# Kernel optimization log

Hardware: AMD Instinct MI355X
Metric: run time of the kernel (lower is better)

Reference implementation:

```python
import jax, jax.numpy as jnp
import numpy as np

N_SYS = 512      # number of crystal systems in the batch
N_ATOM = 32      # atoms per system (uniform for the reference)
N = N_SYS * N_ATOM            # 16384 total atoms
M = N_SYS * N_ATOM * N_ATOM   # 524288 dense intra-system edges
R = 16           # lattice translation points per edge
E = 128          # embed_dim
H = 8            # num_heads


def setup_inputs() -> dict:
    key = jax.random.key(0)
    ks = jax.random.split(key, 6)
    x = jax.random.normal(ks[0], (N, E), jnp.float32)
    in_proj_weight = jax.random.normal(ks[1], (3 * E, E), jnp.float32) / np.float32(np.sqrt(E))
    in_proj_bias = jnp.zeros((3 * E,), jnp.float32)
    out_proj_weight = jax.random.normal(ks[2], (E, E), jnp.float32) / np.float32(np.sqrt(E))
    out_proj_bias = jnp.zeros((E,), jnp.float32)
    # per-node per-head Gaussian exponents; must be negative for convergent lattice sums
    alpha = -(jax.random.uniform(ks[3], (N, H), jnp.float32) * 0.9 + 0.1)
    # squared distances from atom i to lattice images of atom j, up to ~5 Angstrom
    dist2 = jax.random.uniform(ks[4], (M, R), jnp.float32) * 25.0
    # dense intra-system edge list in (query-major) block order, as Crystalformer assumes
    base = (np.arange(N_SYS, dtype=np.int32) * N_ATOM)[:, None, None]
    qi = np.arange(N_ATOM, dtype=np.int32)[None, :, None]
    kj = np.arange(N_ATOM, dtype=np.int32)[None, None, :]
    e0 = np.broadcast_to(base + qi, (N_SYS, N_ATOM, N_ATOM)).reshape(-1)
    e1 = np.broadcast_to(base + kj, (N_SYS, N_ATOM, N_ATOM)).reshape(-1)
    edges = jnp.asarray(np.stack([e0, e1]), jnp.int32)
    batch = jnp.asarray(np.repeat(np.arange(N_SYS, dtype=np.int32), N_ATOM))
    return {
        "x": x,
        "in_proj_weight": in_proj_weight,
        "in_proj_bias": in_proj_bias,
        "out_proj_weight": out_proj_weight,
        "out_proj_bias": out_proj_bias,
        "alpha": alpha,
        "dist2": dist2,
        "edges": edges,
        "batch": batch,
    }


def reference(x, in_proj_weight, in_proj_bias, out_proj_weight, out_proj_bias,
              alpha, dist2, edges, batch):
    n, e = x.shape
    h = alpha.shape[1]
    dh = e // h
    # in-projection (self-attention: q = k = v = x)
    qkv = x @ in_proj_weight.T + in_proj_bias           # [N, 3E]
    q, k, v = jnp.split(qkv, 3, axis=-1)
    q = q.reshape(n, h, dh) / jnp.sqrt(jnp.asarray(dh, x.dtype))
    k = k.reshape(n, h, dh)
    v = v.reshape(n, h, dh)
    e0, e1 = edges[0], edges[1]
    # per-edge dot-product score, gathered q/k  -> [M, H]
    attn = jnp.einsum("mhd,mhd->mh", q[e0], k[e1])
    # real-domain lattice-sum attention bias: logsumexp_r(alpha_i * |r|^2)  -> [M, H]
    aw = jax.nn.logsumexp(alpha[e0][:, :, None] * dist2[:, None, :], axis=-1)
    s = attn + aw
    # segment softmax over each query's neighborhood (norm_func_mode=0 'default')
    smax = jax.ops.segment_max(s, e0, num_segments=n)   # [N, H]
    p = jnp.exp(s - smax[e0])
    denom = jax.ops.segment_sum(p, e0, num_segments=n)  # [N, H]
    p = p / denom[e0]
    # scatter-add aggregation of gathered values  -> [N, H, dh]
    out = jax.ops.segment_sum(p[:, :, None] * v[e1], e0, num_segments=n)
    # out-projection
    out = out.reshape(n, e) @ out_proj_weight.T + out_proj_bias
    return out
```

## Files before the change

kernel.cpp:

```cpp
#include <hip/hip_runtime.h>
#include <hip/hip_bf16.h>

#define LOG2E_F 1.4426950408889634f

typedef __attribute__((ext_vector_type(8))) short short8;
typedef __attribute__((ext_vector_type(4))) float f32x4;
typedef __attribute__((ext_vector_type(2))) float f32x2;

__device__ inline unsigned short f2b(float f) {
    __hip_bfloat16 h = __float2bfloat16(f);
    return *reinterpret_cast<unsigned short*>(&h);
}

__device__ inline short8 load_frag_f32(const float* p) {
    const float4 lo = *(const float4*)p;
    const float4 hi = *(const float4*)(p + 4);
    short8 r;
    r[0] = (short)f2b(lo.x); r[1] = (short)f2b(lo.y);
    r[2] = (short)f2b(lo.z); r[3] = (short)f2b(lo.w);
    r[4] = (short)f2b(hi.x); r[5] = (short)f2b(hi.y);
    r[6] = (short)f2b(hi.z); r[7] = (short)f2b(hi.w);
    return r;
}

__device__ inline f32x2 mk2(float a, float b) { f32x2 r; r.x = a; r.y = b; return r; }
__device__ inline f32x2 bfup(unsigned u) {
    return mk2(__uint_as_float(u << 16), __uint_as_float(u & 0xffff0000u));
}
#define PK_FMA(a, b, c) __builtin_elementwise_fma((a), (b), (c))

__global__ __launch_bounds__(256) void prep_kernel(
    const float* __restrict__ x, const float* __restrict__ Win,
    const float* __restrict__ Wout,
    unsigned short* __restrict__ xbf, unsigned short* __restrict__ winbf,
    unsigned short* __restrict__ woutbf)
{
    const int i = blockIdx.x * 256 + threadIdx.x;
    const float* src; unsigned short* dst; size_t off;
    if (i < 262144)       { src = x;    dst = xbf;    off = (size_t)i * 8; }
    else if (i < 268288)  { src = Win;  dst = winbf;  off = (size_t)(i - 262144) * 8; }
    else                  { src = Wout; dst = woutbf; off = (size_t)(i - 268288) * 8; }
    const short8 r = load_frag_f32(src + off);
    *(short8*)(dst + off) = r;
}

__global__ __launch_bounds__(512, 2) void fused2_kernel(
    const unsigned short* __restrict__ xbf, const unsigned short* __restrict__ winbf,
    const float* __restrict__ bin, const unsigned short* __restrict__ woutbf,
    const float* __restrict__ bout, const float* __restrict__ alpha,
    const float* __restrict__ dist2, float* __restrict__ out)
{
    __shared__ float qf[2][32][164];
    __shared__ unsigned short kvb[2][2][32][8][16];
    __shared__ unsigned short aggb[2][32][136];

    const int tid  = threadIdx.x;
    const int g    = tid >> 8;
    const int t    = tid & 255;
    const int sys  = blockIdx.x * 2 + g;
    const int lane = t & 63;
    const int wv   = t >> 6;
    const int r16  = lane & 15;
    const int kg   = lane >> 4;
    const int base = sys << 5;

    short8 af[2][4];
    #pragma unroll
    for (int rt = 0; rt < 2; ++rt)
        #pragma unroll
        for (int ks = 0; ks < 4; ++ks)
            af[rt][ks] = *(const short8*)(
                xbf + (size_t)(base + rt * 16 + r16) * 128 + ks * 32 + kg * 8);

    #pragma unroll
    for (int j = 0; j < 6; ++j) {
        const int ct = wv * 6 + j;
        const int c  = ct * 16 + r16;
        short8 bf[4];
        #pragma unroll
        for (int ks = 0; ks < 4; ++ks)
            bf[ks] = *(const short8*)(winbf + (size_t)c * 128 + ks * 32 + kg * 8);
        const float bias_v = bin[c];
        const int   bufi   = ct >> 3;
        const int   hh     = ct & 7;

        #pragma unroll
        for (int rt = 0; rt < 2; ++rt) {
            f32x4 acc = {0.f, 0.f, 0.f, 0.f};
            #pragma unroll
            for (int ks = 0; ks < 4; ++ks)
                acc = __builtin_amdgcn_mfma_f32_16x16x32_bf16(af[rt][ks], bf[ks], acc, 0, 0, 0);
            #pragma unroll
            for (int r = 0; r < 4; ++r) {
                const int atom = rt * 16 + kg * 4 + r;
                const float v  = acc[r] + bias_v;
                if (bufi == 0)
                    qf[g][atom][hh * 20 + r16] = v * (0.25f * LOG2E_F);
                else
                    kvb[g][bufi - 1][atom][hh][r16] = f2b(v);
            }
        }
    }

    const int qi = t >> 3;
    const int h  = t & 7;
    const float al2 = alpha[(size_t)(base + qi) * 8 + h] * LOG2E_F;
    const f32x2 al22 = mk2(al2, al2);

    __syncthreads();

    f32x2 q2[8];
    {
        const float* qrow = &qf[g][qi][h * 20];
        #pragma unroll
        for (int d4 = 0; d4 < 4; ++d4) {
            const float4 tq = *(const float4*)(qrow + (d4 << 2));
            q2[d4 * 2 + 0] = mk2(tq.x, tq.y);
            q2[d4 * 2 + 1] = mk2(tq.z, tq.w);
        }
    }

    float den = 0.f;
    f32x2 acc2[8] = {};
    const float* dp = dist2 + (size_t)(sys * 1024 + qi * 32) * 16;

    #pragma unroll 4
    for (int kj = 0; kj < 32; ++kj, dp += 16) {
        const float4 t0 = *(const float4*)(dp + 0);
        const float4 t1 = *(const float4*)(dp + 4);
        const float4 t2 = *(const float4*)(dp + 8);
        const float4 t3 = *(const float4*)(dp + 12);
        const f32x2 d2p[8] = {mk2(t0.x,t0.y), mk2(t0.z,t0.w), mk2(t1.x,t1.y), mk2(t1.z,t1.w),
                              mk2(t2.x,t2.y), mk2(t2.z,t2.w), mk2(t3.x,t3.y), mk2(t3.z,t3.w)};
        f32x2 es;
        {
            const f32x2 a0 = al22 * d2p[0];
            es = mk2(__builtin_amdgcn_exp2f(a0.x), __builtin_amdgcn_exp2f(a0.y));
            #pragma unroll
            for (int i = 1; i < 8; ++i) {
                const f32x2 a = al22 * d2p[i];
                es += mk2(__builtin_amdgcn_exp2f(a.x), __builtin_amdgcn_exp2f(a.y));
            }
        }
        const float ssum = es.x + es.y;

        const uint4* krp = (const uint4*)&kvb[g][0][kj][h][0];
        const uint4 ka = krp[0];
        const uint4 kb = krp[1];
        f32x2 dA = q2[0] * bfup(ka.x);
        f32x2 dB = q2[1] * bfup(ka.y);
        dA = PK_FMA(q2[2], bfup(ka.z), dA);
        dB = PK_FMA(q2[3], bfup(ka.w), dB);
        dA = PK_FMA(q2[4], bfup(kb.x), dA);
        dB = PK_FMA(q2[5], bfup(kb.y), dB);
        dA = PK_FMA(q2[6], bfup(kb.z), dA);
        dB = PK_FMA(q2[7], bfup(kb.w), dB);
        const float dot = (dA.x + dA.y) + (dB.x + dB.y);

        const float p = __builtin_amdgcn_exp2f(dot - 16.0f) * ssum;
        den += p;
        const f32x2 p2 = mk2(p, p);

        const uint4* vrp = (const uint4*)&kvb[g][1][kj][h][0];
        const uint4 va = vrp[0];
        const uint4 vb = vrp[1];
        acc2[0] = PK_FMA(p2, bfup(va.x), acc2[0]);
        acc2[1] = PK_FMA(p2, bfup(va.y), acc2[1]);
        acc2[2] = PK_FMA(p2, bfup(va.z), acc2[2]);
        acc2[3] = PK_FMA(p2, bfup(va.w), acc2[3]);
        acc2[4] = PK_FMA(p2, bfup(vb.x), acc2[4]);
        acc2[5] = PK_FMA(p2, bfup(vb.y), acc2[5]);
        acc2[6] = PK_FMA(p2, bfup(vb.z), acc2[6]);
        acc2[7] = PK_FMA(p2, bfup(vb.w), acc2[7]);
    }

    {
        const float inv = 1.0f / den;
        const f32x2 inv2 = mk2(inv, inv);
        unsigned short* op = &aggb[g][qi][h * 16];
        uint4 o0, o1;
        f32x2 r0 = acc2[0] * inv2, r1 = acc2[1] * inv2;
        f32x2 r2 = acc2[2] * inv2, r3 = acc2[3] * inv2;
        f32x2 r4 = acc2[4] * inv2, r5 = acc2[5] * inv2;
        f32x2 r6 = acc2[6] * inv2, r7 = acc2[7] * inv2;
        o0.x = (unsigned)f2b(r0.x) | ((unsigned)f2b(r0.y) << 16);
        o0.y = (unsigned)f2b(r1.x) | ((unsigned)f2b(r1.y) << 16);
        o0.z = (unsigned)f2b(r2.x) | ((unsigned)f2b(r2.y) << 16);
        o0.w = (unsigned)f2b(r3.x) | ((unsigned)f2b(r3.y) << 16);
        o1.x = (unsigned)f2b(r4.x) | ((unsigned)f2b(r4.y) << 16);
        o1.y = (unsigned)f2b(r5.x) | ((unsigned)f2b(r5.y) << 16);
        o1.z = (unsigned)f2b(r6.x) | ((unsigned)f2b(r6.y) << 16);
        o1.w = (unsigned)f2b(r7.x) | ((unsigned)f2b(r7.y) << 16);
        *(uint4*)op       = o0;
        *(uint4*)(op + 8) = o1;
    }

    __syncthreads();

    short8 aA[2][4];
    #pragma unroll
    for (int rt = 0; rt < 2; ++rt)
        #pragma unroll
        for (int ks = 0; ks < 4; ++ks)
            aA[rt][ks] = *(const short8*)(&aggb[g][rt * 16 + r16][ks * 32 + kg * 8]);

    #pragma unroll
    for (int j = 0; j < 2; ++j) {
        const int ct = wv * 2 + j;
        const int c  = ct * 16 + r16;
        short8 bf[4];
        #pragma unroll
        for (int ks = 0; ks < 4; ++ks)
            bf[ks] = *(const short8*)(woutbf + (size_t)c * 128 + ks * 32 + kg * 8);
        const float bias_v = bout[c];
        #pragma unroll
        for (int rt = 0; rt < 2; ++rt) {
            f32x4 oacc = {0.f, 0.f, 0.f, 0.f};
            #pragma unroll
            for (int ks = 0; ks < 4; ++ks)
                oacc = __builtin_amdgcn_mfma_f32_16x16x32_bf16(aA[rt][ks], bf[ks], oacc, 0, 0, 0);
            #pragma unroll
            for (int r = 0; r < 4; ++r) {
                const int row = base + rt * 16 + kg * 4 + r;
                out[(size_t)row * 128 + c] = oacc[r] + bias_v;
            }
        }
    }
}

extern "C" void kernel_launch(void* const* d_in, const int* in_sizes, int n_in,
                              void* d_out, int out_size, void* d_ws, size_t ws_size,
                              hipStream_t stream)
{
    const float* x     = (const float*)d_in[0];
    const float* Win   = (const float*)d_in[1];
    const float* bin   = (const float*)d_in[2];
    const float* Wout  = (const float*)d_in[3];
    const float* bout  = (const float*)d_in[4];
    const float* alpha = (const float*)d_in[5];
    const float* dist2 = (const float*)d_in[6];

    unsigned short* xbf    = (unsigned short*)d_ws;
    unsigned short* winbf  = xbf + (size_t)16384 * 128;
    unsigned short* woutbf = winbf + (size_t)384 * 128;

    prep_kernel<<<dim3(1056), 256, 0, stream>>>(x, Win, Wout, xbf, winbf, woutbf);
    fused2_kernel<<<dim3(256), 512, 0, stream>>>(
        xbf, winbf, bin, woutbf, bout, alpha, dist2, (float*)d_out);
}
```

Measured before the change: 36.61 us.

## Compute QK scores and PV aggregation with MFMA instead of scalar packed FMAs

Replaces the per-thread scalar dot products and value accumulation in the attention stage with bf16 MFMA instructions. Q and K are stored as zero-padded bf16 rows and V is stored transposed. Probabilities are staged through a per-wave LDS scratch buffer so they can feed a second MFMA. Each block now handles one system with 256 threads instead of two systems with 512. The change trades a large amount of VALU work for extra LDS traffic and shuffles, and lowers q and p precision to bf16.

```diff
diff --git a/kernel.cpp b/kernel.cpp
--- a/kernel.cpp
+++ b/kernel.cpp
@@ -24,10 +24,6 @@
 }
 
 __device__ inline f32x2 mk2(float a, float b) { f32x2 r; r.x = a; r.y = b; return r; }
-__device__ inline f32x2 bfup(unsigned u) {
-    return mk2(__uint_as_float(u << 16), __uint_as_float(u & 0xffff0000u));
-}
-#define PK_FMA(a, b, c) __builtin_elementwise_fma((a), (b), (c))
 
 __global__ __launch_bounds__(256) void prep_kernel(
     const float* __restrict__ x, const float* __restrict__ Win,
@@ -44,42 +40,54 @@
     *(short8*)(dst + off) = r;
 }
 
-__global__ __launch_bounds__(512, 2) void fused2_kernel(
+__global__ __launch_bounds__(256, 2) void fused_mfma_kernel(
     const unsigned short* __restrict__ xbf, const unsigned short* __restrict__ winbf,
     const float* __restrict__ bin, const unsigned short* __restrict__ woutbf,
     const float* __restrict__ bout, const float* __restrict__ alpha,
     const float* __restrict__ dist2, float* __restrict__ out)
 {
-    __shared__ float qf[2][32][164];
-    __shared__ unsigned short kvb[2][2][32][8][16];
-    __shared__ unsigned short aggb[2][32][136];
-
+    __shared__ unsigned short Ql[32][264];
+    __shared__ unsigned short Kl[32][264];
+    __shared__ unsigned short Vt[8][16][40];
+    __shared__ unsigned short pscr[4][32][36];
+    __shared__ float alpha_l[32][8];
+    __shared__ unsigned short aggl[32][136];
+
+    const int sys  = blockIdx.x;
     const int tid  = threadIdx.x;
-    const int g    = tid >> 8;
-    const int t    = tid & 255;
-    const int sys  = blockIdx.x * 2 + g;
-    const int lane = t & 63;
-    const int wv   = t >> 6;
-    const int r16  = lane & 15;
-    const int kg   = lane >> 4;
+    const int lane = tid & 63;
+    const int wv   = tid >> 6;
+    const int c16  = lane & 15;
+    const int g    = lane >> 4;
     const int base = sys << 5;
 
+    {
+        const int atom = tid >> 3;
+        const int hh   = tid & 7;
+        const uint4 z = {0, 0, 0, 0};
+        *(uint4*)&Ql[atom][hh * 32 + 16] = z;
+        *(uint4*)&Ql[atom][hh * 32 + 24] = z;
+        *(uint4*)&Kl[atom][hh * 32 + 16] = z;
+        *(uint4*)&Kl[atom][hh * 32 + 24] = z;
+        alpha_l[atom][hh] = alpha[(size_t)(base + atom) * 8 + hh];
+    }
+
     short8 af[2][4];
     #pragma unroll
     for (int rt = 0; rt < 2; ++rt)
         #pragma unroll
         for (int ks = 0; ks < 4; ++ks)
             af[rt][ks] = *(const short8*)(
-                xbf + (size_t)(base + rt * 16 + r16) * 128 + ks * 32 + kg * 8);
+                xbf + (size_t)(base + rt * 16 + c16) * 128 + ks * 32 + g * 8);
 
     #pragma unroll
     for (int j = 0; j < 6; ++j) {
         const int ct = wv * 6 + j;
-        const int c  = ct * 16 + r16;
+        const int c  = ct * 16 + c16;
         short8 bf[4];
         #pragma unroll
         for (int ks = 0; ks < 4; ++ks)
-            bf[ks] = *(const short8*)(winbf + (size_t)c * 128 + ks * 32 + kg * 8);
+            bf[ks] = *(const short8*)(winbf + (size_t)c * 128 + ks * 32 + g * 8);
         const float bias_v = bin[c];
         const int   bufi   = ct >> 3;
         const int   hh     = ct & 7;
@@ -92,107 +100,107 @@
                 acc = __builtin_amdgcn_mfma_f32_16x16x32_bf16(af[rt][ks], bf[ks], acc, 0, 0, 0);
             #pragma unroll
             for (int r = 0; r < 4; ++r) {
-                const int atom = rt * 16 + kg * 4 + r;
+                const int atom = rt * 16 + g * 4 + r;
                 const float v  = acc[r] + bias_v;
                 if (bufi == 0)
-                    qf[g][atom][hh * 20 + r16] = v * (0.25f * LOG2E_F);
+                    Ql[atom][hh * 32 + c16] = f2b(v * (0.25f * LOG2E_F));
+                else if (bufi == 1)
+                    Kl[atom][hh * 32 + c16] = f2b(v);
                 else
-                    kvb[g][bufi - 1][atom][hh][r16] = f2b(v);
-            }
-        }
-    }
-
-    const int qi = t >> 3;
-    const int h  = t & 7;
-    const float al2 = alpha[(size_t)(base + qi) * 8 + h] * LOG2E_F;
-    const f32x2 al22 = mk2(al2, al2);
+                    Vt[hh][c16][atom] = f2b(v);
+            }
+        }
+    }
 
     __syncthreads();
 
-    f32x2 q2[8];
-    {
-        const float* qrow = &qf[g][qi][h * 20];
-        #pragma unroll
-        for (int d4 = 0; d4 < 4; ++d4) {
-            const float4 tq = *(const float4*)(qrow + (d4 << 2));
-            q2[d4 * 2 + 0] = mk2(tq.x, tq.y);
-            q2[d4 * 2 + 1] = mk2(tq.z, tq.w);
-        }
-    }
-
-    float den = 0.f;
-    f32x2 acc2[8] = {};
-    const float* dp = dist2 + (size_t)(sys * 1024 + qi * 32) * 16;
-
-    #pragma unroll 4
-    for (int kj = 0; kj < 32; ++kj, dp += 16) {
-        const float4 t0 = *(const float4*)(dp + 0);
-        const float4 t1 = *(const float4*)(dp + 4);
-        const float4 t2 = *(const float4*)(dp + 8);
-        const float4 t3 = *(const float4*)(dp + 12);
-        const f32x2 d2p[8] = {mk2(t0.x,t0.y), mk2(t0.z,t0.w), mk2(t1.x,t1.y), mk2(t1.z,t1.w),
-                              mk2(t2.x,t2.y), mk2(t2.z,t2.w), mk2(t3.x,t3.y), mk2(t3.z,t3.w)};
-        f32x2 es;
-        {
-            const f32x2 a0 = al22 * d2p[0];
-            es = mk2(__builtin_amdgcn_exp2f(a0.x), __builtin_amdgcn_exp2f(a0.y));
-            #pragma unroll
-            for (int i = 1; i < 8; ++i) {
-                const f32x2 a = al22 * d2p[i];
-                es += mk2(__builtin_amdgcn_exp2f(a.x), __builtin_amdgcn_exp2f(a.y));
-            }
-        }
-        const float ssum = es.x + es.y;
-
-        const uint4* krp = (const uint4*)&kvb[g][0][kj][h][0];
-        const uint4 ka = krp[0];
-        const uint4 kb = krp[1];
-        f32x2 dA = q2[0] * bfup(ka.x);
-        f32x2 dB = q2[1] * bfup(ka.y);
-        dA = PK_FMA(q2[2], bfup(ka.z), dA);
-        dB = PK_FMA(q2[3], bfup(ka.w), dB);
-        dA = PK_FMA(q2[4], bfup(kb.x), dA);
-        dB = PK_FMA(q2[5], bfup(kb.y), dB);
-        dA = PK_FMA(q2[6], bfup(kb.z), dA);
-        dB = PK_FMA(q2[7], bfup(kb.w), dB);
-        const float dot = (dA.x + dA.y) + (dB.x + dB.y);
-
-        const float p = __builtin_amdgcn_exp2f(dot - 16.0f) * ssum;
-        den += p;
-        const f32x2 p2 = mk2(p, p);
-
-        const uint4* vrp = (const uint4*)&kvb[g][1][kj][h][0];
-        const uint4 va = vrp[0];
-        const uint4 vb = vrp[1];
-        acc2[0] = PK_FMA(p2, bfup(va.x), acc2[0]);
-        acc2[1] = PK_FMA(p2, bfup(va.y), acc2[1]);
-        acc2[2] = PK_FMA(p2, bfup(va.z), acc2[2]);
-        acc2[3] = PK_FMA(p2, bfup(va.w), acc2[3]);
-        acc2[4] = PK_FMA(p2, bfup(vb.x), acc2[4]);
-        acc2[5] = PK_FMA(p2, bfup(vb.y), acc2[5]);
-        acc2[6] = PK_FMA(p2, bfup(vb.z), acc2[6]);
-        acc2[7] = PK_FMA(p2, bfup(vb.w), acc2[7]);
-    }
-
-    {
-        const float inv = 1.0f / den;
-        const f32x2 inv2 = mk2(inv, inv);
-        unsigned short* op = &aggb[g][qi][h * 16];
-        uint4 o0, o1;
-        f32x2 r0 = acc2[0] * inv2, r1 = acc2[1] * inv2;
-        f32x2 r2 = acc2[2] * inv2, r3 = acc2[3] * inv2;
-        f32x2 r4 = acc2[4] * inv2, r5 = acc2[5] * inv2;
-        f32x2 r6 = acc2[6] * inv2, r7 = acc2[7] * inv2;
-        o0.x = (unsigned)f2b(r0.x) | ((unsigned)f2b(r0.y) << 16);
-        o0.y = (unsigned)f2b(r1.x) | ((unsigned)f2b(r1.y) << 16);
-        o0.z = (unsigned)f2b(r2.x) | ((unsigned)f2b(r2.y) << 16);
-        o0.w = (unsigned)f2b(r3.x) | ((unsigned)f2b(r3.y) << 16);
-        o1.x = (unsigned)f2b(r4.x) | ((unsigned)f2b(r4.y) << 16);
-        o1.y = (unsigned)f2b(r5.x) | ((unsigned)f2b(r5.y) << 16);
-        o1.z = (unsigned)f2b(r6.x) | ((unsigned)f2b(r6.y) << 16);
-        o1.w = (unsigned)f2b(r7.x) | ((unsigned)f2b(r7.y) << 16);
-        *(uint4*)op       = o0;
-        *(uint4*)(op + 8) = o1;
+    const f32x4 zero4 = {0.f, 0.f, 0.f, 0.f};
+    #pragma unroll
+    for (int hh2 = 0; hh2 < 2; ++hh2) {
+        const int h = wv * 2 + hh2;
+
+        short8 kA0 = *(const short8*)&Kl[c16][h * 32 + g * 8];
+        short8 kA1 = *(const short8*)&Kl[c16 + 16][h * 32 + g * 8];
+        short8 qB0 = *(const short8*)&Ql[c16][h * 32 + g * 8];
+        short8 qB1 = *(const short8*)&Ql[c16 + 16][h * 32 + g * 8];
+        f32x4 st[2][2];
+        st[0][0] = __builtin_amdgcn_mfma_f32_16x16x32_bf16(kA0, qB0, zero4, 0, 0, 0);
+        st[0][1] = __builtin_amdgcn_mfma_f32_16x16x32_bf16(kA0, qB1, zero4, 0, 0, 0);
+        st[1][0] = __builtin_amdgcn_mfma_f32_16x16x32_bf16(kA1, qB0, zero4, 0, 0, 0);
+        st[1][1] = __builtin_amdgcn_mfma_f32_16x16x32_bf16(kA1, qB1, zero4, 0, 0, 0);
+
+        const float al2q0 = alpha_l[c16][h] * LOG2E_F;
+        const float al2q1 = alpha_l[c16 + 16][h] * LOG2E_F;
+        const float* bq0 = dist2 + ((size_t)(base + c16) * 32 + g * 4) * 16;
+        const float* bq1 = dist2 + ((size_t)(base + c16 + 16) * 32 + g * 4) * 16;
+
+        float p[2][2][4];
+        float den0 = 0.f, den1 = 0.f;
+
+        #pragma unroll
+        for (int qt = 0; qt < 2; ++qt) {
+            const float  al2  = qt ? al2q1 : al2q0;
+            const f32x2  a2   = mk2(al2, al2);
+            const float* bq   = qt ? bq1 : bq0;
+            #pragma unroll
+            for (int kt = 0; kt < 2; ++kt) {
+                #pragma unroll
+                for (int r = 0; r < 4; ++r) {
+                    const float* dp = bq + (r + 16 * kt) * 16;
+                    const float4 t0 = *(const float4*)(dp + 0);
+                    const float4 t1 = *(const float4*)(dp + 4);
+                    const float4 t2 = *(const float4*)(dp + 8);
+                    const float4 t3 = *(const float4*)(dp + 12);
+                    const f32x2 d2p[8] = {mk2(t0.x,t0.y), mk2(t0.z,t0.w),
+                                          mk2(t1.x,t1.y), mk2(t1.z,t1.w),
+                                          mk2(t2.x,t2.y), mk2(t2.z,t2.w),
+                                          mk2(t3.x,t3.y), mk2(t3.z,t3.w)};
+                    f32x2 es;
+                    {
+                        const f32x2 a0 = a2 * d2p[0];
+                        es = mk2(__builtin_amdgcn_exp2f(a0.x), __builtin_amdgcn_exp2f(a0.y));
+                        #pragma unroll
+                        for (int i = 1; i < 8; ++i) {
+                            const f32x2 a = a2 * d2p[i];
+                            es += mk2(__builtin_amdgcn_exp2f(a.x), __builtin_amdgcn_exp2f(a.y));
+                        }
+                    }
+                    const float ssum = es.x + es.y;
+                    const float pv = __builtin_amdgcn_exp2f(st[kt][qt][r] - 16.0f) * ssum;
+                    p[kt][qt][r] = pv;
+                    if (qt == 0) den0 += pv; else den1 += pv;
+                }
+            }
+        }
+
+        den0 += __shfl_xor(den0, 16); den0 += __shfl_xor(den0, 32);
+        den1 += __shfl_xor(den1, 16); den1 += __shfl_xor(den1, 32);
+
+        #pragma unroll
+        for (int qt = 0; qt < 2; ++qt) {
+            const int q = c16 + 16 * qt;
+            #pragma unroll
+            for (int kt = 0; kt < 2; ++kt) {
+                uint2 w;
+                w.x = (unsigned)f2b(p[kt][qt][0]) | ((unsigned)f2b(p[kt][qt][1]) << 16);
+                w.y = (unsigned)f2b(p[kt][qt][2]) | ((unsigned)f2b(p[kt][qt][3]) << 16);
+                *(uint2*)&pscr[wv][q][kt * 16 + g * 4] = w;
+            }
+        }
+
+        const short8 vA  = *(const short8*)&Vt[h][c16][g * 8];
+        const short8 pB0 = *(const short8*)&pscr[wv][c16][g * 8];
+        const short8 pB1 = *(const short8*)&pscr[wv][c16 + 16][g * 8];
+        const f32x4 ov0 = __builtin_amdgcn_mfma_f32_16x16x32_bf16(vA, pB0, zero4, 0, 0, 0);
+        const f32x4 ov1 = __builtin_amdgcn_mfma_f32_16x16x32_bf16(vA, pB1, zero4, 0, 0, 0);
+
+        const float inv0 = 1.0f / den0;
+        const float inv1 = 1.0f / den1;
+        #pragma unroll
+        for (int r = 0; r < 4; ++r) {
+            aggl[c16][h * 16 + g * 4 + r]      = f2b(ov0[r] * inv0);
+            aggl[c16 + 16][h * 16 + g * 4 + r] = f2b(ov1[r] * inv1);
+        }
     }
 
     __syncthreads();
@@ -202,16 +210,16 @@
     for (int rt = 0; rt < 2; ++rt)
         #pragma unroll
         for (int ks = 0; ks < 4; ++ks)
-            aA[rt][ks] = *(const short8*)(&aggb[g][rt * 16 + r16][ks * 32 + kg * 8]);
+            aA[rt][ks] = *(const short8*)&aggl[rt * 16 + c16][ks * 32 + g * 8];
 
     #pragma unroll
     for (int j = 0; j < 2; ++j) {
         const int ct = wv * 2 + j;
-        const int c  = ct * 16 + r16;
+        const int c  = ct * 16 + c16;
         short8 bf[4];
         #pragma unroll
         for (int ks = 0; ks < 4; ++ks)
-            bf[ks] = *(const short8*)(woutbf + (size_t)c * 128 + ks * 32 + kg * 8);
+            bf[ks] = *(const short8*)(woutbf + (size_t)c * 128 + ks * 32 + g * 8);
         const float bias_v = bout[c];
         #pragma unroll
         for (int rt = 0; rt < 2; ++rt) {
@@ -221,7 +229,7 @@
                 oacc = __builtin_amdgcn_mfma_f32_16x16x32_bf16(aA[rt][ks], bf[ks], oacc, 0, 0, 0);
             #pragma unroll
             for (int r = 0; r < 4; ++r) {
-                const int row = base + rt * 16 + kg * 4 + r;
+                const int row = base + rt * 16 + g * 4 + r;
                 out[(size_t)row * 128 + c] = oacc[r] + bias_v;
             }
         }
@@ -245,6 +253,6 @@
     unsigned short* woutbf = winbf + (size_t)384 * 128;
 
     prep_kernel<<<dim3(1056), 256, 0, stream>>>(x, Win, Wout, xbf, winbf, woutbf);
-    fused2_kernel<<<dim3(256), 512, 0, stream>>>(
+    fused_mfma_kernel<<<dim3(512), 256, 0, stream>>>(
         xbf, winbf, bin, woutbf, bout, alpha, dist2, (float*)d_out);
 }
```

After: 70.63 us. +92.9%, slower.

## Compute P·V aggregation with MFMA using transposed V and staged probabilities

Applied to the files above, without the earlier changes.

Replaces the per-thread scalar packed-FMA accumulation of p*V with a matrix-core pass. Probabilities are packed to bf16 into a shared scratch buffer, and V is stored transposed in shared memory. Each wave then runs 16x16x32 bf16 MFMAs per head and applies the reciprocal denominator before writing the aggregate. The score loop is also fully unrolled. This adds an extra barrier, more shared memory and bf16 rounding of the probabilities, while cutting the per-edge VALU work.

```diff
diff --git a/kernel.cpp b/kernel.cpp
--- a/kernel.cpp
+++ b/kernel.cpp
@@ -50,14 +50,17 @@
     const float* __restrict__ bout, const float* __restrict__ alpha,
     const float* __restrict__ dist2, float* __restrict__ out)
 {
-    __shared__ float qf[2][32][164];
-    __shared__ unsigned short kvb[2][2][32][8][16];
-    __shared__ unsigned short aggb[2][32][136];
+    __shared__ float          qf[2][32][164];
+    __shared__ unsigned short Kb[2][32][8][16];
+    __shared__ unsigned short Vt[2][8][16][40];
+    __shared__ unsigned short pscr[2][8][33][40];
+    __shared__ float          denl[2][8][33];
+    __shared__ unsigned short aggl[2][32][136];
 
     const int tid  = threadIdx.x;
-    const int g    = tid >> 8;
+    const int grp  = tid >> 8;
     const int t    = tid & 255;
-    const int sys  = blockIdx.x * 2 + g;
+    const int sys  = blockIdx.x * 2 + grp;
     const int lane = t & 63;
     const int wv   = t >> 6;
     const int r16  = lane & 15;
@@ -95,9 +98,11 @@
                 const int atom = rt * 16 + kg * 4 + r;
                 const float v  = acc[r] + bias_v;
                 if (bufi == 0)
-                    qf[g][atom][hh * 20 + r16] = v * (0.25f * LOG2E_F);
+                    qf[grp][atom][hh * 20 + r16] = v * (0.25f * LOG2E_F);
+                else if (bufi == 1)
+                    Kb[grp][atom][hh][r16] = f2b(v);
                 else
-                    kvb[g][bufi - 1][atom][hh][r16] = f2b(v);
+                    Vt[grp][hh][r16][atom] = f2b(v);
             }
         }
     }
@@ -111,7 +116,7 @@
 
     f32x2 q2[8];
     {
-        const float* qrow = &qf[g][qi][h * 20];
+        const float* qrow = &qf[grp][qi][h * 20];
         #pragma unroll
         for (int d4 = 0; d4 < 4; ++d4) {
             const float4 tq = *(const float4*)(qrow + (d4 << 2));
@@ -121,15 +126,17 @@
     }
 
     float den = 0.f;
-    f32x2 acc2[8] = {};
+    unsigned pw[16];
+    float plo = 0.f;
     const float* dp = dist2 + (size_t)(sys * 1024 + qi * 32) * 16;
 
-    #pragma unroll 4
-    for (int kj = 0; kj < 32; ++kj, dp += 16) {
-        const float4 t0 = *(const float4*)(dp + 0);
-        const float4 t1 = *(const float4*)(dp + 4);
-        const float4 t2 = *(const float4*)(dp + 8);
-        const float4 t3 = *(const float4*)(dp + 12);
+    #pragma unroll
+    for (int kj = 0; kj < 32; ++kj) {
+        const float* dpk = dp + kj * 16;
+        const float4 t0 = *(const float4*)(dpk + 0);
+        const float4 t1 = *(const float4*)(dpk + 4);
+        const float4 t2 = *(const float4*)(dpk + 8);
+        const float4 t3 = *(const float4*)(dpk + 12);
         const f32x2 d2p[8] = {mk2(t0.x,t0.y), mk2(t0.z,t0.w), mk2(t1.x,t1.y), mk2(t1.z,t1.w),
                               mk2(t2.x,t2.y), mk2(t2.z,t2.w), mk2(t3.x,t3.y), mk2(t3.z,t3.w)};
         f32x2 es;
@@ -144,9 +151,8 @@
         }
         const float ssum = es.x + es.y;
 
-        const uint4* krp = (const uint4*)&kvb[g][0][kj][h][0];
-        const uint4 ka = krp[0];
-        const uint4 kb = krp[1];
+        const uint4 ka = *(const uint4*)&Kb[grp][kj][h][0];
+        const uint4 kb = *(const uint4*)&Kb[grp][kj][h][8];
         f32x2 dA = q2[0] * bfup(ka.x);
         f32x2 dB = q2[1] * bfup(ka.y);
         dA = PK_FMA(q2[2], bfup(ka.z), dA);
@@ -159,50 +165,53 @@
 
         const float p = __builtin_amdgcn_exp2f(dot - 16.0f) * ssum;
         den += p;
-        const f32x2 p2 = mk2(p, p);
-
-        const uint4* vrp = (const uint4*)&kvb[g][1][kj][h][0];
-        const uint4 va = vrp[0];
-        const uint4 vb = vrp[1];
-        acc2[0] = PK_FMA(p2, bfup(va.x), acc2[0]);
-        acc2[1] = PK_FMA(p2, bfup(va.y), acc2[1]);
-        acc2[2] = PK_FMA(p2, bfup(va.z), acc2[2]);
-        acc2[3] = PK_FMA(p2, bfup(va.w), acc2[3]);
-        acc2[4] = PK_FMA(p2, bfup(vb.x), acc2[4]);
-        acc2[5] = PK_FMA(p2, bfup(vb.y), acc2[5]);
-        acc2[6] = PK_FMA(p2, bfup(vb.z), acc2[6]);
-        acc2[7] = PK_FMA(p2, bfup(vb.w), acc2[7]);
+
+        if ((kj & 1) == 0) {
+            plo = p;
+        } else {
+            pw[kj >> 1] = (unsigned)f2b(plo) | ((unsigned)f2b(p) << 16);
+        }
     }
 
     {
-        const float inv = 1.0f / den;
-        const f32x2 inv2 = mk2(inv, inv);
-        unsigned short* op = &aggb[g][qi][h * 16];
-        uint4 o0, o1;
-        f32x2 r0 = acc2[0] * inv2, r1 = acc2[1] * inv2;
-        f32x2 r2 = acc2[2] * inv2, r3 = acc2[3] * inv2;
-        f32x2 r4 = acc2[4] * inv2, r5 = acc2[5] * inv2;
-        f32x2 r6 = acc2[6] * inv2, r7 = acc2[7] * inv2;
-        o0.x = (unsigned)f2b(r0.x) | ((unsigned)f2b(r0.y) << 16);
-        o0.y = (unsigned)f2b(r1.x) | ((unsigned)f2b(r1.y) << 16);
-        o0.z = (unsigned)f2b(r2.x) | ((unsigned)f2b(r2.y) << 16);
-        o0.w = (unsigned)f2b(r3.x) | ((unsigned)f2b(r3.y) << 16);
-        o1.x = (unsigned)f2b(r4.x) | ((unsigned)f2b(r4.y) << 16);
-        o1.y = (unsigned)f2b(r5.x) | ((unsigned)f2b(r5.y) << 16);
-        o1.z = (unsigned)f2b(r6.x) | ((unsigned)f2b(r6.y) << 16);
-        o1.w = (unsigned)f2b(r7.x) | ((unsigned)f2b(r7.y) << 16);
-        *(uint4*)op       = o0;
-        *(uint4*)(op + 8) = o1;
+        unsigned short* pr = &pscr[grp][h][qi][0];
+        *(uint4*)(pr + 0)  = *(uint4*)&pw[0];
+        *(uint4*)(pr + 8)  = *(uint4*)&pw[4];
+        *(uint4*)(pr + 16) = *(uint4*)&pw[8];
+        *(uint4*)(pr + 24) = *(uint4*)&pw[12];
+        denl[grp][h][qi] = 1.0f / den;
     }
 
     __syncthreads();
 
+    const f32x4 zero4 = {0.f, 0.f, 0.f, 0.f};
+    #pragma unroll
+    for (int hh2 = 0; hh2 < 2; ++hh2) {
+        const int hh = wv * 2 + hh2;
+        const short8 vA  = *(const short8*)&Vt[grp][hh][r16][kg * 8];
+        const short8 pB0 = *(const short8*)&pscr[grp][hh][r16][kg * 8];
+        const short8 pB1 = *(const short8*)&pscr[grp][hh][r16 + 16][kg * 8];
+        const f32x4 o0 = __builtin_amdgcn_mfma_f32_16x16x32_bf16(vA, pB0, zero4, 0, 0, 0);
+        const f32x4 o1 = __builtin_amdgcn_mfma_f32_16x16x32_bf16(vA, pB1, zero4, 0, 0, 0);
+        const float inv0 = denl[grp][hh][r16];
+        const float inv1 = denl[grp][hh][r16 + 16];
+        uint2 w0, w1;
+        w0.x = (unsigned)f2b(o0[0] * inv0) | ((unsigned)f2b(o0[1] * inv0) << 16);
+        w0.y = (unsigned)f2b(o0[2] * inv0) | ((unsigned)f2b(o0[3] * inv0) << 16);
+        w1.x = (unsigned)f2b(o1[0] * inv1) | ((unsigned)f2b(o1[1] * inv1) << 16);
+        w1.y = (unsigned)f2b(o1[2] * inv1) | ((unsigned)f2b(o1[3] * inv1) << 16);
+        *(uint2*)&aggl[grp][r16][hh * 16 + kg * 4]      = w0;
+        *(uint2*)&aggl[grp][r16 + 16][hh * 16 + kg * 4] = w1;
+    }
+
+    __syncthreads();
+
     short8 aA[2][4];
     #pragma unroll
     for (int rt = 0; rt < 2; ++rt)
         #pragma unroll
         for (int ks = 0; ks < 4; ++ks)
-            aA[rt][ks] = *(const short8*)(&aggb[g][rt * 16 + r16][ks * 32 + kg * 8]);
+            aA[rt][ks] = *(const short8*)&aggl[grp][rt * 16 + r16][ks * 32 + kg * 8];
 
     #pragma unroll
     for (int j = 0; j < 2; ++j) {
```

After: 35.95 us (median of 2 runs). Within noise of the previous version (-1.8%).
